# Performance work log

Hardware: AMD Instinct MI355X
Metric: run time of the kernel (lower is better)

Reference implementation:

```python
import jax, jax.numpy as jnp
import numpy as np

SH_C0 = 0.28209479177387814
SH_C1 = 0.4886025119029199


def quat_to_rot(q):
    # q: [..., 4] in (w, x, y, z) order, as in 3DGS
    q = q / jnp.linalg.norm(q, axis=-1, keepdims=True)
    w, x, y, z = q[..., 0], q[..., 1], q[..., 2], q[..., 3]
    R = jnp.stack([
        1 - 2 * (y * y + z * z), 2 * (x * y - w * z), 2 * (x * z + w * y),
        2 * (x * y + w * z), 1 - 2 * (x * x + z * z), 2 * (y * z - w * x),
        2 * (x * z - w * y), 2 * (y * z + w * x), 1 - 2 * (x * x + y * y)],
        axis=-1)
    return R.reshape(q.shape[:-1] + (3, 3))


def _render_one_view(xyz, feats, cov3d, opacity, c2w, intr, H, W):
    # xyz [N,3], feats [N,4,3], cov3d [N,3,3], opacity [N], c2w [4,4], intr [4]
    w2c = jnp.linalg.inv(c2w)
    Rcw, tcw = w2c[:3, :3], w2c[:3, 3]
    p = xyz @ Rcw.T + tcw                     # camera-space means [N,3]
    x, y, z = p[:, 0], p[:, 1], p[:, 2]
    valid = z > 0.2                           # near-plane cull
    zs = jnp.maximum(z, 0.2)
    fx, fy, cx, cy = intr[0], intr[1], intr[2], intr[3]
    u = fx * x / zs + cx                      # pixel-space 2D means
    v = fy * y / zs + cy
    # EWA projection Jacobian [N,2,3]
    zero = jnp.zeros_like(zs)
    J = jnp.stack([fx / zs, zero, -fx * x / (zs * zs),
                   zero, fy / zs, -fy * y / (zs * zs)], axis=-1).reshape(-1, 2, 3)
    cov_cam = jnp.einsum('ij,njk,lk->nil', Rcw, cov3d, Rcw)
    cov2d = jnp.einsum('nij,njk,nlk->nil', J, cov_cam, J)
    a = cov2d[:, 0, 0] + 0.3                  # low-pass dilation as in 3DGS
    b = cov2d[:, 0, 1]
    c = cov2d[:, 1, 1] + 0.3
    det = jnp.maximum(a * c - b * b, 1e-6)
    ca, cb, cc = c / det, -b / det, a / det   # conic (inverse 2x2 cov)
    # SH degree-1 color from view direction
    campos = c2w[:3, 3]
    d = xyz - campos
    d = d / jnp.linalg.norm(d, axis=-1, keepdims=True)
    color = (SH_C0 * feats[:, 0]
             - SH_C1 * d[:, 1:2] * feats[:, 1]
             + SH_C1 * d[:, 2:3] * feats[:, 2]
             - SH_C1 * d[:, 0:1] * feats[:, 3]) + 0.5
    color = jnp.maximum(color, 0.0)
    op = jnp.where(valid, opacity, 0.0)
    # global front-to-back depth sort (reference for the tiled sort)
    order = jnp.argsort(jnp.where(valid, z, jnp.inf))
    u, v = u[order], v[order]
    ca, cb, cc = ca[order], cb[order], cc[order]
    color, op = color[order], op[order]
    # pixel centers
    px = jnp.arange(W, dtype=xyz.dtype) + 0.5
    py = jnp.arange(H, dtype=xyz.dtype) + 0.5
    gx, gy = jnp.meshgrid(px, py)             # [H,W], gx varies along W
    dx = gx.reshape(-1, 1) - u[None, :]       # [P,N]
    dy = gy.reshape(-1, 1) - v[None, :]
    power = -0.5 * (ca * dx * dx + cc * dy * dy) - cb * dx * dy
    alpha = jnp.where(power > 0, 0.0,
                      jnp.minimum(0.99, op * jnp.exp(jnp.minimum(power, 0.0))))
    alpha = jnp.where(alpha < 1.0 / 255.0, 0.0, alpha)
    T = jnp.cumprod(1.0 - alpha, axis=-1)
    T_prev = jnp.concatenate([jnp.ones_like(T[:, :1]), T[:, :-1]], axis=-1)
    wgt = alpha * T_prev                      # [P,N] composite weights
    img = wgt @ color                         # [P,3]
    return img.reshape(H, W, 3).transpose(2, 0, 1)


def setup_inputs() -> dict:
    key = jax.random.key(0)
    ks = jax.random.split(key, 5)
    b, n, H, W = 1, 1024, 128, 128
    xyz = jax.random.normal(ks[0], (b, n, 3), dtype=jnp.float32)
    features = jax.random.normal(ks[1], (b, n, 4, 3), dtype=jnp.float32) * 0.5
    scaling = 0.01 + 0.06 * jax.random.uniform(ks[2], (b, n, 3), dtype=jnp.float32)
    rotation = jax.random.normal(ks[3], (b, n, 4), dtype=jnp.float32)
    opacity = jax.random.uniform(ks[4], (b, n, 1), dtype=jnp.float32)
    # two OpenCV cameras at radius 3 looking at the origin
    def make_c2w(angle):
        ca, sa = np.cos(angle), np.sin(angle)
        Ry = np.array([[ca, 0, sa], [0, 1, 0], [-sa, 0, ca]], dtype=np.float32)
        M = np.eye(4, dtype=np.float32)
        M[:3, :3] = Ry
        M[:3, 3] = Ry @ np.array([0.0, 0.0, -3.0], dtype=np.float32)
        return M
    C2W = jnp.asarray(np.stack([make_c2w(0.0), make_c2w(0.4)])[None])  # [1,2,4,4]
    intr = np.array([float(W), float(W), W / 2.0, H / 2.0], dtype=np.float32)
    fxfycxcy = jnp.asarray(np.broadcast_to(intr, (b, 2, 4)).copy())
    return {"xyz": xyz, "features": features, "scaling": scaling,
            "rotation": rotation, "opacity": opacity,
            "height": H, "width": W, "C2W": C2W, "fxfycxcy": fxfycxcy}


def reference(xyz, features, scaling, rotation, opacity, height, width, C2W, fxfycxcy):
    H, W = int(height), int(width)
    R = quat_to_rot(rotation)                  # [b,N,3,3]
    M = R * scaling[..., None, :]
    cov3d = M @ jnp.swapaxes(M, -1, -2)        # [b,N,3,3]
    op = opacity[..., 0]
    def per_batch(xyz_b, f_b, cov_b, op_b, c2w_b, intr_b):
        return jax.vmap(lambda c2w, intr: _render_one_view(
            xyz_b, f_b, cov_b, op_b, c2w, intr, H, W))(c2w_b, intr_b)
    return jax.vmap(per_batch)(xyz, features, cov3d, op, C2W, fxfycxcy)  # [b,v,3,H,W]
```

## Files before the change

### kernel.cpp

```cpp
#include <hip/hip_runtime.h>
#include <math.h>

#define NG 1024
#define HH 128
#define WW 128
#define NV 2
#define SH_C0 0.28209479177387814f
#define SH_C1 0.4886025119029199f

#define RECF 12
#define REC_SORT 0

#define TILE 16
#define TPX  (WW/TILE)
#define TPY  (HH/TILE)
#define NT   (TPX*TPY)
#define RCH  128

__global__ __launch_bounds__(256) void prep_rank_kernel(
    const float* __restrict__ xyz, const float* __restrict__ feats,
    const float* __restrict__ scaling, const float* __restrict__ rotation,
    const float* __restrict__ opacity, const float* __restrict__ C2W,
    const float* __restrict__ intr, float* __restrict__ ws)
{
    __shared__ unsigned long long s_key[NG];
    __shared__ int s_cnt[256];

    const int iv  = blockIdx.x >> 3;
    const int seg = blockIdx.x & 7;
    const int t   = threadIdx.x;

    const float* c2w = C2W + iv * 16;
    const float r20 = c2w[2], r21 = c2w[6], r22 = c2w[10];
    const float tc2 = -(r20*c2w[3] + r21*c2w[7] + r22*c2w[11]);

    #pragma unroll
    for (int k = 0; k < 4; ++k) {
        const int g = k*256 + t;
        const float X = xyz[g*3+0], Y = xyz[g*3+1], Z = xyz[g*3+2];
        const float pz = r20*X + r21*Y + r22*Z + tc2;
        const float zk = (pz > 0.2f) ? pz : 100000.0f;
        s_key[g] = (((unsigned long long)__float_as_uint(zk)) << 10)
                 | (unsigned long long)(unsigned)g;
    }
    __syncthreads();

    const int g    = seg*128 + (t & 127);
    const int half = t >> 7;
    const unsigned long long ki = s_key[g];
    {
        const unsigned long long* kp = s_key + half*512;
        int cnt = 0;
        #pragma unroll 8
        for (int j = 0; j < 512; ++j)
            cnt += (kp[j] < ki) ? 1 : 0;
        s_cnt[t] = cnt;
    }
    __syncthreads();

    if (t >= 128) return;
    const int rank = s_cnt[t] + s_cnt[t+128];

    const float fx = intr[iv*4+0], fy = intr[iv*4+1];
    const float cx = intr[iv*4+2], cy = intr[iv*4+3];

    float Rcw[3][3], tcw[3];
    #pragma unroll
    for (int r = 0; r < 3; ++r)
        #pragma unroll
        for (int c = 0; c < 3; ++c)
            Rcw[r][c] = c2w[c*4 + r];
    #pragma unroll
    for (int r = 0; r < 3; ++r)
        tcw[r] = -(Rcw[r][0]*c2w[3] + Rcw[r][1]*c2w[7] + Rcw[r][2]*c2w[11]);
    const float camx = c2w[3], camy = c2w[7], camz = c2w[11];

    const float X = xyz[g*3+0], Y = xyz[g*3+1], Z = xyz[g*3+2];

    float qw = rotation[g*4+0], qx = rotation[g*4+1];
    float qy = rotation[g*4+2], qz = rotation[g*4+3];
    const float qn = rsqrtf(qw*qw + qx*qx + qy*qy + qz*qz);
    qw *= qn; qx *= qn; qy *= qn; qz *= qn;
    const float R00 = 1.f - 2.f*(qy*qy + qz*qz);
    const float R01 = 2.f*(qx*qy - qw*qz);
    const float R02 = 2.f*(qx*qz + qw*qy);
    const float R10 = 2.f*(qx*qy + qw*qz);
    const float R11 = 1.f - 2.f*(qx*qx + qz*qz);
    const float R12 = 2.f*(qy*qz - qw*qx);
    const float R20 = 2.f*(qx*qz - qw*qy);
    const float R21 = 2.f*(qy*qz + qw*qx);
    const float R22 = 1.f - 2.f*(qx*qx + qy*qy);

    const float s0 = scaling[g*3+0], s1 = scaling[g*3+1], s2 = scaling[g*3+2];
    const float M00 = R00*s0, M01 = R01*s1, M02 = R02*s2;
    const float M10 = R10*s0, M11 = R11*s1, M12 = R12*s2;
    const float M20 = R20*s0, M21 = R21*s1, M22 = R22*s2;

    const float S00 = M00*M00 + M01*M01 + M02*M02;
    const float S01 = M00*M10 + M01*M11 + M02*M12;
    const float S02 = M00*M20 + M01*M21 + M02*M22;
    const float S11 = M10*M10 + M11*M11 + M12*M12;
    const float S12 = M10*M20 + M11*M21 + M12*M22;
    const float S22 = M20*M20 + M21*M21 + M22*M22;

    float tmp[3][3];
    const float S[3][3] = {{S00,S01,S02},{S01,S11,S12},{S02,S12,S22}};
    #pragma unroll
    for (int r = 0; r < 3; ++r)
        #pragma unroll
        for (int c = 0; c < 3; ++c)
            tmp[r][c] = Rcw[r][0]*S[0][c] + Rcw[r][1]*S[1][c] + Rcw[r][2]*S[2][c];
    float C[3][3];
    #pragma unroll
    for (int r = 0; r < 3; ++r)
        #pragma unroll
        for (int c = 0; c < 3; ++c)
            C[r][c] = tmp[r][0]*Rcw[c][0] + tmp[r][1]*Rcw[c][1] + tmp[r][2]*Rcw[c][2];

    const float px_ = Rcw[0][0]*X + Rcw[0][1]*Y + Rcw[0][2]*Z + tcw[0];
    const float py_ = Rcw[1][0]*X + Rcw[1][1]*Y + Rcw[1][2]*Z + tcw[1];
    const float zf  = __uint_as_float((unsigned)(ki >> 10));
    const bool valid = zf < 99999.0f;

    const float zs = fmaxf(zf, 0.2f);
    const float izs = 1.f / zs;

    const float u = fx*px_*izs + cx;
    const float v = fy*py_*izs + cy;

    const float a00 = fx*izs;
    const float a02 = -fx*px_*izs*izs;
    const float a11 = fy*izs;
    const float a12 = -fy*py_*izs*izs;

    const float c00 = a00*a00*C[0][0] + 2.f*a00*a02*C[0][2] + a02*a02*C[2][2] + 0.3f;
    const float c01 = a00*a11*C[0][1] + a00*a12*C[0][2] + a02*a11*C[1][2] + a02*a12*C[2][2];
    const float c11 = a11*a11*C[1][1] + 2.f*a11*a12*C[1][2] + a12*a12*C[2][2] + 0.3f;

    const float det = fmaxf(c00*c11 - c01*c01, 1e-6f);
    const float idet = 1.f / det;

    float dx = X - camx, dy = Y - camy, dz = Z - camz;
    const float dn = rsqrtf(dx*dx + dy*dy + dz*dz);
    dx *= dn; dy *= dn; dz *= dn;
    const float* f = feats + g*12;
    float col[3];
    #pragma unroll
    for (int c = 0; c < 3; ++c) {
        float cc_ = SH_C0*f[0*3+c] - SH_C1*dy*f[1*3+c] + SH_C1*dz*f[2*3+c]
                    - SH_C1*dx*f[3*3+c] + 0.5f;
        col[c] = fmaxf(cc_, 0.f);
    }

    const float op = valid ? opacity[g] : 0.f;
    const float pwmin = -logf(255.f * op);

    const float Aq = -0.5f * (c11*idet);
    const float Bq = c01*idet;
    const float Cq = -0.5f * (c00*idet);

    float dumax = -1.f, dvmax = -1.f;
    if (op >= (1.f/255.f)) {
        const float L = -pwmin;
        dumax = sqrtf(2.f*L*c00);
        dvmax = sqrtf(2.f*L*c11);
    }

    float4* dst = (float4*)(ws + REC_SORT + (size_t)(iv*NG + rank)*RECF);
    dst[0] = make_float4(u,  v,  Aq,    Bq);
    dst[1] = make_float4(Cq, pwmin, op, col[0]);
    dst[2] = make_float4(col[1], col[2], dumax, dvmax);
}

__global__ __launch_bounds__(256) void render_kernel(
    const float* __restrict__ ws, float* __restrict__ out)
{
    __shared__ unsigned short s_ids[NG];
    __shared__ int s_scan[256];
    __shared__ float4 s_rec[RCH*3];

    const int iv   = blockIdx.x / NT;
    const int tile = blockIdx.x % NT;
    const int tx0  = (tile % TPX) * TILE;
    const int ty0  = (tile / TPX) * TILE;
    const int t    = threadIdx.x;

    const float xlo = tx0 + 0.5f, xhi = tx0 + TILE - 0.5f;
    const float ylo = ty0 + 0.5f, yhi = ty0 + TILE - 0.5f;

    const float4* recs = (const float4*)(ws + REC_SORT + (size_t)iv*NG*3*4/4*0)
                       + (size_t)iv*NG*3;

    int flags = 0, cnt = 0;
    #pragma unroll
    for (int k = 0; k < 4; ++k) {
        const int gidx = t*4 + k;
        const float4 g0 = recs[gidx*3+0];
        const float4 g2 = recs[gidx*3+2];
        const bool hit = (g0.x - g2.z <= xhi) && (g0.x + g2.z >= xlo)
                      && (g0.y - g2.w <= yhi) && (g0.y + g2.w >= ylo)
                      && (g2.z >= 0.f);
        flags |= (hit ? 1 : 0) << k;
        cnt   += hit ? 1 : 0;
    }
    s_scan[t] = cnt;
    __syncthreads();

    #pragma unroll
    for (int d = 1; d < 256; d <<= 1) {
        const int vv = (t >= d) ? s_scan[t-d] : 0;
        __syncthreads();
        s_scan[t] += vv;
        __syncthreads();
    }
    int base = s_scan[t] - cnt;
    const int m = s_scan[255];
    #pragma unroll
    for (int k = 0; k < 4; ++k) {
        if (flags & (1 << k)) s_ids[base++] = (unsigned short)(t*4 + k);
    }
    __syncthreads();

    const int px = tx0 + (t & (TILE-1));
    const int py = ty0 + (t >> 4);
    const float gx = px + 0.5f;
    const float gy = py + 0.5f;

    float T = 1.f, ar = 0.f, ag = 0.f, ab = 0.f;

    for (int c0 = 0; c0 < m; c0 += RCH) {
        const int nc = min(RCH, m - c0);
        for (int idx = t; idx < nc*3; idx += 256) {
            const int rid = s_ids[c0 + idx/3];
            s_rec[idx] = recs[rid*3 + idx%3];
        }
        __syncthreads();

        if (T >= 1e-5f) {
            for (int j = 0; j < nc; ++j) {
                const float4 g0 = s_rec[j*3+0];
                const float4 g1 = s_rec[j*3+1];
                const float du = gx - g0.x;
                const float dv = gy - g0.y;
                const float pw = fmaf(g0.z, du*du, fmaf(g1.x, dv*dv, g0.w*(du*dv)));
                if (pw <= 0.f && pw >= g1.y) {
                    const float al = fminf(0.99f, g1.z * __expf(pw));
                    if (al >= (1.f/255.f)) {
                        const float4 g2 = s_rec[j*3+2];
                        const float w = al * T;
                        ar += w * g1.w;
                        ag += w * g2.x;
                        ab += w * g2.y;
                        T *= (1.f - al);
                        if (T < 1e-5f) break;
                    }
                }
            }
        }
        __syncthreads();
    }

    out[((iv*3 + 0)*HH + py)*WW + px] = ar;
    out[((iv*3 + 1)*HH + py)*WW + px] = ag;
    out[((iv*3 + 2)*HH + py)*WW + px] = ab;
}

extern "C" void kernel_launch(void* const* d_in, const int* in_sizes, int n_in,
                              void* d_out, int out_size, void* d_ws, size_t ws_size,
                              hipStream_t stream) {
    const float* xyz      = (const float*)d_in[0];
    const float* feats    = (const float*)d_in[1];
    const float* scaling  = (const float*)d_in[2];
    const float* rotation = (const float*)d_in[3];
    const float* opacity  = (const float*)d_in[4];
    const float* C2W      = (const float*)d_in[7];
    const float* intr     = (const float*)d_in[8];

    float* ws  = (float*)d_ws;
    float* out = (float*)d_out;

    prep_rank_kernel<<<NV*8, 256, 0, stream>>>(
        xyz, feats, scaling, rotation, opacity, C2W, intr, ws);

    render_kernel<<<NV*NT, 256, 0, stream>>>(ws, out);
}
```

Before: 89.47 us.

## Repack gaussian records, use wave-shuffle scan, and enlarge render chunk

Reorders the per-gaussian record so the tile-culling test reads only the first float4 (mean plus extents), halving global loads in the culling pass. Replaces the 256-entry shared-memory Hillis-Steele scan, with its many block barriers, by a 64-lane shuffle scan plus a 4-wave combine. Doubles the shared-memory record chunk to 256 so fewer load/sync rounds are needed. The larger LDS footprint may reduce occupancy.

```diff
diff --git a/kernel.cpp b/kernel.cpp
--- a/kernel.cpp
+++ b/kernel.cpp
@@ -9,13 +9,13 @@
 #define SH_C1 0.4886025119029199f
 
 #define RECF 12
-#define REC_SORT 0
 
 #define TILE 16
 #define TPX  (WW/TILE)
 #define TPY  (HH/TILE)
 #define NT   (TPX*TPY)
-#define RCH  128
+#define RCH  256
+
 
 __global__ __launch_bounds__(256) void prep_rank_kernel(
     const float* __restrict__ xyz, const float* __restrict__ feats,
@@ -166,17 +166,17 @@
         dvmax = sqrtf(2.f*L*c11);
     }
 
-    float4* dst = (float4*)(ws + REC_SORT + (size_t)(iv*NG + rank)*RECF);
-    dst[0] = make_float4(u,  v,  Aq,    Bq);
-    dst[1] = make_float4(Cq, pwmin, op, col[0]);
-    dst[2] = make_float4(col[1], col[2], dumax, dvmax);
+    float4* dst = (float4*)(ws + (size_t)(iv*NG + rank)*RECF);
+    dst[0] = make_float4(u,  v,  dumax, dvmax);
+    dst[1] = make_float4(Aq, Bq, Cq,    pwmin);
+    dst[2] = make_float4(op, col[0], col[1], col[2]);
 }
 
 __global__ __launch_bounds__(256) void render_kernel(
     const float* __restrict__ ws, float* __restrict__ out)
 {
     __shared__ unsigned short s_ids[NG];
-    __shared__ int s_scan[256];
+    __shared__ int s_wsum[4];
     __shared__ float4 s_rec[RCH*3];
 
     const int iv   = blockIdx.x / NT;
@@ -184,37 +184,40 @@
     const int tx0  = (tile % TPX) * TILE;
     const int ty0  = (tile / TPX) * TILE;
     const int t    = threadIdx.x;
+    const int lane = t & 63;
+    const int wid  = t >> 6;
 
     const float xlo = tx0 + 0.5f, xhi = tx0 + TILE - 0.5f;
     const float ylo = ty0 + 0.5f, yhi = ty0 + TILE - 0.5f;
 
-    const float4* recs = (const float4*)(ws + REC_SORT + (size_t)iv*NG*3*4/4*0)
-                       + (size_t)iv*NG*3;
+    const float4* recs = (const float4*)ws + (size_t)iv*NG*3;
 
     int flags = 0, cnt = 0;
     #pragma unroll
     for (int k = 0; k < 4; ++k) {
         const int gidx = t*4 + k;
         const float4 g0 = recs[gidx*3+0];
-        const float4 g2 = recs[gidx*3+2];
-        const bool hit = (g0.x - g2.z <= xhi) && (g0.x + g2.z >= xlo)
-                      && (g0.y - g2.w <= yhi) && (g0.y + g2.w >= ylo)
-                      && (g2.z >= 0.f);
+        const bool hit = (g0.z >= 0.f)
+                      && (g0.x - g0.z <= xhi) && (g0.x + g0.z >= xlo)
+                      && (g0.y - g0.w <= yhi) && (g0.y + g0.w >= ylo);
         flags |= (hit ? 1 : 0) << k;
         cnt   += hit ? 1 : 0;
     }
-    s_scan[t] = cnt;
-    __syncthreads();
-
-    #pragma unroll
-    for (int d = 1; d < 256; d <<= 1) {
-        const int vv = (t >= d) ? s_scan[t-d] : 0;
-        __syncthreads();
-        s_scan[t] += vv;
-        __syncthreads();
-    }
-    int base = s_scan[t] - cnt;
-    const int m = s_scan[255];
+
+    int v = cnt;
+    #pragma unroll
+    for (int d = 1; d < 64; d <<= 1) {
+        const int n = __shfl_up(v, d, 64);
+        if (lane >= d) v += n;
+    }
+    if (lane == 63) s_wsum[wid] = v;
+    __syncthreads();
+    int waveOff = 0;
+    #pragma unroll
+    for (int w = 0; w < 4; ++w)
+        if (w < wid) waveOff += s_wsum[w];
+    const int m = s_wsum[0] + s_wsum[1] + s_wsum[2] + s_wsum[3];
+    int base = waveOff + v - cnt;
     #pragma unroll
     for (int k = 0; k < 4; ++k) {
         if (flags & (1 << k)) s_ids[base++] = (unsigned short)(t*4 + k);
@@ -242,15 +245,15 @@
                 const float4 g1 = s_rec[j*3+1];
                 const float du = gx - g0.x;
                 const float dv = gy - g0.y;
-                const float pw = fmaf(g0.z, du*du, fmaf(g1.x, dv*dv, g0.w*(du*dv)));
-                if (pw <= 0.f && pw >= g1.y) {
-                    const float al = fminf(0.99f, g1.z * __expf(pw));
+                const float pw = fmaf(g1.x, du*du, fmaf(g1.z, dv*dv, g1.y*(du*dv)));
+                if (pw <= 0.f && pw >= g1.w) {
+                    const float4 g2 = s_rec[j*3+2];
+                    const float al = fminf(0.99f, g2.x * __expf(pw));
                     if (al >= (1.f/255.f)) {
-                        const float4 g2 = s_rec[j*3+2];
                         const float w = al * T;
-                        ar += w * g1.w;
-                        ag += w * g2.x;
-                        ab += w * g2.y;
+                        ar += w * g2.y;
+                        ag += w * g2.z;
+                        ab += w * g2.w;
                         T *= (1.f - al);
                         if (T < 1e-5f) break;
                     }
```

Measured after the change: 88.60 us. No clear change (-1.0%).
